# Kernel optimization log

Hardware: AMD Instinct MI355X
Metric: run time of the kernel (lower is better)

The kernel has to match this reference:

```python
import jax, jax.numpy as jnp
import numpy as np

B = 262144
I = 128  # input_size
H = 128  # hidden_size


def setup_inputs() -> dict:
    key = jax.random.key(0)
    ks = jax.random.split(key, 12)
    std = 1.0 / np.sqrt(H)
    u = lambda k, shape: jax.random.uniform(k, shape, jnp.float32, -std, std)
    return {
        "inputs": jax.random.normal(ks[0], (B, I), jnp.float32),
        "h_prev": jax.random.normal(ks[1], (B, H), jnp.float32),
        "c_prev": jax.random.normal(ks[2], (B, H), jnp.float32),
        "W_ii": u(ks[3], (H, I)), "W_hi": u(ks[4], (H, H)),
        "W_if": u(ks[5], (H, I)), "W_hf": u(ks[6], (H, H)),
        "W_io": u(ks[7], (H, I)), "W_ho": u(ks[8], (H, H)),
        "W_ig": u(ks[9], (H, I)), "W_hg": u(ks[10], (H, H)),
    }


def reference(inputs, h_prev, c_prev, W_ii, W_hi, W_if, W_hf, W_io, W_ho, W_ig, W_hg):
    # Same math as 8 separate GEMMs, expressed as 2 fused GEMMs over concatenated gates.
    W_x = jnp.concatenate([W_ii, W_if, W_io, W_ig], axis=0)  # [4H, I]
    W_h = jnp.concatenate([W_hi, W_hf, W_ho, W_hg], axis=0)  # [4H, H]
    gates = inputs @ W_x.T + h_prev @ W_h.T  # [B, 4H]
    gi, gf, go, gg = jnp.split(gates, 4, axis=-1)
    i_t = jax.nn.sigmoid(gi)
    f_t = jax.nn.sigmoid(gf)
    o_t = jax.nn.sigmoid(go)
    g_t = jnp.tanh(gg)
    c_t = f_t * c_prev + i_t * g_t
    h_t = o_t * jnp.tanh(c_t)
    return jnp.stack([h_t, c_t], axis=0)  # [2, B, H]
```

## Files before the change

kernel.cpp:

```cpp
#include <hip/hip_runtime.h>

#define BATCH 262144
#define NBLK 256
#define NITER 16
#define ASTRIDE 264
#define BH 33554432

typedef __attribute__((ext_vector_type(8))) short bf16x8;
typedef __attribute__((ext_vector_type(4))) float f32x4;
typedef __attribute__((ext_vector_type(8))) unsigned short u16x8;

__device__ __forceinline__ unsigned short f2bf(float f) {
  unsigned int u = __float_as_uint(f);
  u += 0x7fffu + ((u >> 16) & 1u);
  return (unsigned short)(u >> 16);
}

__device__ __forceinline__ float fexp(float x) { return __builtin_amdgcn_exp2f(x * 1.44269504f); }
__device__ __forceinline__ float sigm(float x) { return __builtin_amdgcn_rcpf(1.f + fexp(-x)); }
__device__ __forceinline__ float ftanh(float x) { return 1.f - 2.f * __builtin_amdgcn_rcpf(1.f + fexp(2.f * x)); }

__global__ __launch_bounds__(512, 2) void lstm_fused(
    const float* __restrict__ X, const float* __restrict__ H0, const float* __restrict__ C0,
    const float* __restrict__ Wii, const float* __restrict__ Whi,
    const float* __restrict__ Wif, const float* __restrict__ Whf,
    const float* __restrict__ Wio, const float* __restrict__ Who,
    const float* __restrict__ Wig, const float* __restrict__ Whg,
    float* __restrict__ Out) {
  __shared__ __align__(16) unsigned short Abuf[2][64 * ASTRIDE];

  const int tid = threadIdx.x;
  const int wave = tid >> 6;
  const int lane = tid & 63;
  const int lrow = lane & 15;
  const int lk = (lane >> 4) * 8;
  const int hcol = wave * 16 + lrow;
  const int r0 = tid >> 4;
  const int cc = (tid & 15) * 8;

  const float* Wxp[4] = {Wii, Wif, Wio, Wig};
  const float* Whp[4] = {Whi, Whf, Who, Whg};

  bf16x8 wf[4][8];
#pragma unroll
  for (int g = 0; g < 4; ++g) {
#pragma unroll
    for (int kk = 0; kk < 8; ++kk) {
      const int k = kk * 32 + lk;
      const float* src = (kk < 4) ? (Wxp[g] + hcol * 128 + k)
                                  : (Whp[g] + hcol * 128 + (k - 128));
      float4 lo = *(const float4*)src;
      float4 hi = *(const float4*)(src + 4);
      bf16x8 w;
      w[0] = (short)f2bf(lo.x); w[1] = (short)f2bf(lo.y);
      w[2] = (short)f2bf(lo.z); w[3] = (short)f2bf(lo.w);
      w[4] = (short)f2bf(hi.x); w[5] = (short)f2bf(hi.y);
      w[6] = (short)f2bf(hi.z); w[7] = (short)f2bf(hi.w);
      wf[g][kk] = w;
    }
  }

  float4 sx0, sx1, sx2, sx3, sh0, sh1, sh2, sh3;
  float cv[16];

#define ISSUE_LOADS(ROW0) do {                                           \
    const float* px_ = X + (size_t)((ROW0) + r0) * 128 + cc;             \
    sx0 = *(const float4*)px_;  sx1 = *(const float4*)(px_ + 4);         \
    const float* ph_ = H0 + (size_t)((ROW0) + r0) * 128 + cc;            \
    sh0 = *(const float4*)ph_;  sh1 = *(const float4*)(ph_ + 4);         \
    const float* qx_ = px_ + 32 * 128;                                   \
    sx2 = *(const float4*)qx_;  sx3 = *(const float4*)(qx_ + 4);         \
    const float* qh_ = ph_ + 32 * 128;                                   \
    sh2 = *(const float4*)qh_;  sh3 = *(const float4*)(qh_ + 4);         \
  } while (0)

#define ISSUE_CV(ROW0) do {                                              \
    const int rbv_ = (ROW0) + (lane >> 4) * 4;                           \
    _Pragma("unroll")                                                    \
    for (int mt_ = 0; mt_ < 4; ++mt_)                                    \
      _Pragma("unroll")                                                  \
      for (int j_ = 0; j_ < 4; ++j_)                                     \
        cv[mt_ * 4 + j_] = C0[(size_t)(rbv_ + mt_ * 16 + j_) * 128 + hcol]; \
  } while (0)

#define CVT8(DST, A, B) do {                                             \
    u16x8 t_;                                                            \
    t_[0] = f2bf((A).x); t_[1] = f2bf((A).y);                            \
    t_[2] = f2bf((A).z); t_[3] = f2bf((A).w);                            \
    t_[4] = f2bf((B).x); t_[5] = f2bf((B).y);                            \
    t_[6] = f2bf((B).z); t_[7] = f2bf((B).w);                            \
    *(u16x8*)(DST) = t_;                                                 \
  } while (0)

#define BODY(IT, AB) do {                                                \
    const int row0_ = (blockIdx.x + (IT) * NBLK) * 64;                   \
                              \
    CVT8(&(AB)[r0 * ASTRIDE + cc], sx0, sx1);                            \
    CVT8(&(AB)[r0 * ASTRIDE + 128 + cc], sh0, sh1);                      \
    CVT8(&(AB)[(r0 + 32) * ASTRIDE + cc], sx2, sx3);                     \
    CVT8(&(AB)[(r0 + 32) * ASTRIDE + 128 + cc], sh2, sh3);               \
    __syncthreads();        \
    \
        \
                                       \
    ISSUE_CV(row0_);                                                     \
    if ((IT) + 1 < NITER) ISSUE_LOADS(row0_ + NBLK * 64);                \
    const int rb_ = row0_ + (lane >> 4) * 4;                             \
    _Pragma("unroll")                                                    \
    for (int mt = 0; mt < 4; ++mt) {                                     \
      f32x4 a0 = {0.f, 0.f, 0.f, 0.f}, a1 = a0, a2 = a0, a3 = a0;        \
      _Pragma("unroll")                                                  \
      for (int kk = 0; kk < 8; ++kk) {                                   \
        bf16x8 a = *(const bf16x8*)&(AB)[(mt * 16 + lrow) * ASTRIDE + kk * 32 + lk]; \
        a0 = __builtin_amdgcn_mfma_f32_16x16x32_bf16(a, wf[0][kk], a0, 0, 0, 0); \
        a1 = __builtin_amdgcn_mfma_f32_16x16x32_bf16(a, wf[1][kk], a1, 0, 0, 0); \
        a2 = __builtin_amdgcn_mfma_f32_16x16x32_bf16(a, wf[2][kk], a2, 0, 0, 0); \
        a3 = __builtin_amdgcn_mfma_f32_16x16x32_bf16(a, wf[3][kk], a3, 0, 0, 0); \
      }                                                                  \
      _Pragma("unroll")                                                  \
      for (int j = 0; j < 4; ++j) {                                      \
        const int rg = rb_ + mt * 16 + j;                                \
        const float itv = sigm(a0[j]);                                   \
        const float ftv = sigm(a1[j]);                                   \
        const float otv = sigm(a2[j]);                                   \
        const float gtv = ftanh(a3[j]);                                  \
        const float ctv = ftv * cv[mt * 4 + j] + itv * gtv;              \
        const float htv = otv * ftanh(ctv);                              \
        Out[(size_t)rg * 128 + hcol] = htv;                              \
        Out[BH + (size_t)rg * 128 + hcol] = ctv;                         \
      }                                                                  \
    }                                                                    \
  } while (0)

  ISSUE_LOADS(blockIdx.x * 64);

  for (int it = 0; it < NITER; it += 2) {
    BODY(it, &Abuf[0][0]);
    BODY(it + 1, &Abuf[1][0]);
  }

#undef ISSUE_LOADS
#undef ISSUE_CV
#undef CVT8
#undef BODY
}

extern "C" void kernel_launch(void* const* d_in, const int* in_sizes, int n_in,
                              void* d_out, int out_size, void* d_ws, size_t ws_size,
                              hipStream_t stream) {
  (void)in_sizes; (void)n_in; (void)out_size; (void)d_ws; (void)ws_size;
  lstm_fused<<<NBLK, 512, 0, stream>>>(
      (const float*)d_in[0], (const float*)d_in[1], (const float*)d_in[2],
      (const float*)d_in[3], (const float*)d_in[4], (const float*)d_in[5],
      (const float*)d_in[6], (const float*)d_in[7], (const float*)d_in[8],
      (const float*)d_in[9], (const float*)d_in[10],
      (float*)d_out);
}
```

Before: 160.4 us.

## Split hidden columns across blocks and exchange gate results through LDS

Each block now covers 32 rows and half of the hidden columns, and each wave holds weights for only two gates, so register pressure drops and occupancy can rise to four blocks per CU. Gate pre-activations are written to an LDS buffer so every thread can gather all four gates for one column. This gives coalesced 64-wide stores for h and c and coalesced c_prev loads. Block-to-tile mapping is swizzled by XCD. In exchange, each block's X/H tile is loaded twice (once per column half), and every iteration gains an extra barrier plus an LDS round trip.

After: 178.8 us. 1.11x slower.

```diff
diff --git a/kernel.cpp b/kernel.cpp
--- a/kernel.cpp
+++ b/kernel.cpp
@@ -1,9 +1,12 @@
 #include <hip/hip_runtime.h>
 
 #define BATCH 262144
-#define NBLK 256
-#define NITER 16
+#define NBLK 512
+#define NITER 32
+#define ROWS 32
 #define ASTRIDE 264
+#define GSTRIDE 68
+#define GPLANE (ROWS * GSTRIDE)
 #define BH 33554432
 
 typedef __attribute__((ext_vector_type(8))) short bf16x8;
@@ -20,33 +23,43 @@
 __device__ __forceinline__ float sigm(float x) { return __builtin_amdgcn_rcpf(1.f + fexp(-x)); }
 __device__ __forceinline__ float ftanh(float x) { return 1.f - 2.f * __builtin_amdgcn_rcpf(1.f + fexp(2.f * x)); }
 
-__global__ __launch_bounds__(512, 2) void lstm_fused(
+__global__ __launch_bounds__(512, 4) void lstm_fused(
     const float* __restrict__ X, const float* __restrict__ H0, const float* __restrict__ C0,
     const float* __restrict__ Wii, const float* __restrict__ Whi,
     const float* __restrict__ Wif, const float* __restrict__ Whf,
     const float* __restrict__ Wio, const float* __restrict__ Who,
     const float* __restrict__ Wig, const float* __restrict__ Whg,
     float* __restrict__ Out) {
-  __shared__ __align__(16) unsigned short Abuf[2][64 * ASTRIDE];
+  __shared__ __align__(16) unsigned short Abuf[2][ROWS * ASTRIDE];
+  __shared__ __align__(16) float Glds[4 * GPLANE];
 
   const int tid = threadIdx.x;
   const int wave = tid >> 6;
   const int lane = tid & 63;
   const int lrow = lane & 15;
-  const int lk = (lane >> 4) * 8;
-  const int hcol = wave * 16 + lrow;
-  const int r0 = tid >> 4;
-  const int cc = (tid & 15) * 8;
+  const int lkq = lane >> 4;
+  const int ct = wave & 3;
+  const int gp = wave >> 2;
+
+  const int bid = blockIdx.x;
+  const int xcd = bid & 7;
+  const int ch = (bid >> 3) & 1;
+  const int p = bid >> 4;
+  const int tbase = p + 32 * xcd;
+  const int col0 = ch * 64;
+
+  const int hcol = col0 + ct * 16 + lrow;
 
   const float* Wxp[4] = {Wii, Wif, Wio, Wig};
   const float* Whp[4] = {Whi, Whf, Who, Whg};
 
-  bf16x8 wf[4][8];
+  bf16x8 wf[2][8];
 #pragma unroll
-  for (int g = 0; g < 4; ++g) {
+  for (int gg = 0; gg < 2; ++gg) {
+    const int g = gp * 2 + gg;
 #pragma unroll
     for (int kk = 0; kk < 8; ++kk) {
-      const int k = kk * 32 + lk;
+      const int k = kk * 32 + lkq * 8;
       const float* src = (kk < 4) ? (Wxp[g] + hcol * 128 + k)
                                   : (Whp[g] + hcol * 128 + (k - 128));
       float4 lo = *(const float4*)src;
@@ -56,83 +69,89 @@
       w[2] = (short)f2bf(lo.z); w[3] = (short)f2bf(lo.w);
       w[4] = (short)f2bf(hi.x); w[5] = (short)f2bf(hi.y);
       w[6] = (short)f2bf(hi.z); w[7] = (short)f2bf(hi.w);
-      wf[g][kk] = w;
+      wf[gg][kk] = w;
     }
   }
 
-  float4 sx0, sx1, sx2, sx3, sh0, sh1, sh2, sh3;
-  float cv[16];
+  const int r0 = tid >> 4;
+  const int ci = tid & 15;
+  float4 s0, s1, s2, s3;
+  float cva[4];
 
-#define ISSUE_LOADS(ROW0) do {                                           \
-    const float* px_ = X + (size_t)((ROW0) + r0) * 128 + cc;             \
-    sx0 = *(const float4*)px_;  sx1 = *(const float4*)(px_ + 4);         \
-    const float* ph_ = H0 + (size_t)((ROW0) + r0) * 128 + cc;            \
-    sh0 = *(const float4*)ph_;  sh1 = *(const float4*)(ph_ + 4);         \
-    const float* qx_ = px_ + 32 * 128;                                   \
-    sx2 = *(const float4*)qx_;  sx3 = *(const float4*)(qx_ + 4);         \
-    const float* qh_ = ph_ + 32 * 128;                                   \
-    sh2 = *(const float4*)qh_;  sh3 = *(const float4*)(qh_ + 4);         \
+#define ISSUE_LOADS(ROW0) do {                                            \
+    const float* b_ = (ci < 8)                                            \
+        ? (X + (size_t)((ROW0) + r0) * 128 + ci * 16)                     \
+        : (H0 + (size_t)((ROW0) + r0) * 128 + (ci - 8) * 16);             \
+    s0 = ((const float4*)b_)[0];  s1 = ((const float4*)b_)[1];            \
+    s2 = ((const float4*)b_)[2];  s3 = ((const float4*)b_)[3];            \
   } while (0)
 
-#define ISSUE_CV(ROW0) do {                                              \
-    const int rbv_ = (ROW0) + (lane >> 4) * 4;                           \
-    _Pragma("unroll")                                                    \
-    for (int mt_ = 0; mt_ < 4; ++mt_)                                    \
-      _Pragma("unroll")                                                  \
-      for (int j_ = 0; j_ < 4; ++j_)                                     \
-        cv[mt_ * 4 + j_] = C0[(size_t)(rbv_ + mt_ * 16 + j_) * 128 + hcol]; \
+#define ISSUE_CV(ROW0) do {                                               \
+    _Pragma("unroll")                                                     \
+    for (int j_ = 0; j_ < 4; ++j_)                                        \
+      cva[j_] = C0[(size_t)((ROW0) + 4 * wave + j_) * 128 + col0 + lane]; \
   } while (0)
 
-#define CVT8(DST, A, B) do {                                             \
-    u16x8 t_;                                                            \
-    t_[0] = f2bf((A).x); t_[1] = f2bf((A).y);                            \
-    t_[2] = f2bf((A).z); t_[3] = f2bf((A).w);                            \
-    t_[4] = f2bf((B).x); t_[5] = f2bf((B).y);                            \
-    t_[6] = f2bf((B).z); t_[7] = f2bf((B).w);                            \
-    *(u16x8*)(DST) = t_;                                                 \
+#define CVT8(DST, A, B) do {                                              \
+    u16x8 t_;                                                             \
+    t_[0] = f2bf((A).x); t_[1] = f2bf((A).y);                             \
+    t_[2] = f2bf((A).z); t_[3] = f2bf((A).w);                             \
+    t_[4] = f2bf((B).x); t_[5] = f2bf((B).y);                             \
+    t_[6] = f2bf((B).z); t_[7] = f2bf((B).w);                             \
+    *(u16x8*)(DST) = t_;                                                  \
   } while (0)
 
-#define BODY(IT, AB) do {                                                \
-    const int row0_ = (blockIdx.x + (IT) * NBLK) * 64;                   \
-                              \
-    CVT8(&(AB)[r0 * ASTRIDE + cc], sx0, sx1);                            \
-    CVT8(&(AB)[r0 * ASTRIDE + 128 + cc], sh0, sh1);                      \
-    CVT8(&(AB)[(r0 + 32) * ASTRIDE + cc], sx2, sx3);                     \
-    CVT8(&(AB)[(r0 + 32) * ASTRIDE + 128 + cc], sh2, sh3);               \
-    __syncthreads();        \
-    \
-        \
-                                       \
-    ISSUE_CV(row0_);                                                     \
-    if ((IT) + 1 < NITER) ISSUE_LOADS(row0_ + NBLK * 64);                \
-    const int rb_ = row0_ + (lane >> 4) * 4;                             \
-    _Pragma("unroll")                                                    \
-    for (int mt = 0; mt < 4; ++mt) {                                     \
-      f32x4 a0 = {0.f, 0.f, 0.f, 0.f}, a1 = a0, a2 = a0, a3 = a0;        \
-      _Pragma("unroll")                                                  \
-      for (int kk = 0; kk < 8; ++kk) {                                   \
-        bf16x8 a = *(const bf16x8*)&(AB)[(mt * 16 + lrow) * ASTRIDE + kk * 32 + lk]; \
-        a0 = __builtin_amdgcn_mfma_f32_16x16x32_bf16(a, wf[0][kk], a0, 0, 0, 0); \
-        a1 = __builtin_amdgcn_mfma_f32_16x16x32_bf16(a, wf[1][kk], a1, 0, 0, 0); \
-        a2 = __builtin_amdgcn_mfma_f32_16x16x32_bf16(a, wf[2][kk], a2, 0, 0, 0); \
-        a3 = __builtin_amdgcn_mfma_f32_16x16x32_bf16(a, wf[3][kk], a3, 0, 0, 0); \
-      }                                                                  \
-      _Pragma("unroll")                                                  \
-      for (int j = 0; j < 4; ++j) {                                      \
-        const int rg = rb_ + mt * 16 + j;                                \
-        const float itv = sigm(a0[j]);                                   \
-        const float ftv = sigm(a1[j]);                                   \
-        const float otv = sigm(a2[j]);                                   \
-        const float gtv = ftanh(a3[j]);                                  \
-        const float ctv = ftv * cv[mt * 4 + j] + itv * gtv;              \
-        const float htv = otv * ftanh(ctv);                              \
-        Out[(size_t)rg * 128 + hcol] = htv;                              \
-        Out[BH + (size_t)rg * 128 + hcol] = ctv;                         \
-      }                                                                  \
-    }                                                                    \
+#define BODY(IT, AB) do {                                                 \
+    const int row0_ = (tbase + (IT) * 256) * ROWS;                        \
+                                             \
+    CVT8(&(AB)[r0 * ASTRIDE + ci * 16], s0, s1);                          \
+    CVT8(&(AB)[r0 * ASTRIDE + ci * 16 + 8], s2, s3);                      \
+    __syncthreads();    \
+    ISSUE_CV(row0_);          \
+                                  \
+    f32x4 a00 = {0.f, 0.f, 0.f, 0.f}, a01 = a00, a10 = a00, a11 = a00;    \
+    _Pragma("unroll")                                                     \
+    for (int kk = 0; kk < 8; ++kk) {                                      \
+      bf16x8 aA = *(const bf16x8*)&(AB)[lrow * ASTRIDE + kk * 32 + lkq * 8];        \
+      bf16x8 aB = *(const bf16x8*)&(AB)[(16 + lrow) * ASTRIDE + kk * 32 + lkq * 8]; \
+      a00 = __builtin_amdgcn_mfma_f32_16x16x32_bf16(aA, wf[0][kk], a00, 0, 0, 0);   \
+      a01 = __builtin_amdgcn_mfma_f32_16x16x32_bf16(aA, wf[1][kk], a01, 0, 0, 0);   \
+      a10 = __builtin_amdgcn_mfma_f32_16x16x32_bf16(aB, wf[0][kk], a10, 0, 0, 0);   \
+      a11 = __builtin_amdgcn_mfma_f32_16x16x32_bf16(aB, wf[1][kk], a11, 0, 0, 0);   \
+    }                                                                     \
+                                          \
+    _Pragma("unroll")                                                     \
+    for (int j_ = 0; j_ < 4; ++j_) {                                      \
+      const int gr = (lkq * 4 + j_) * GSTRIDE + ct * 16 + lrow;           \
+      Glds[(gp * 2 + 0) * GPLANE + gr] = a00[j_];                         \
+      Glds[(gp * 2 + 1) * GPLANE + gr] = a01[j_];                         \
+      Glds[(gp * 2 + 0) * GPLANE + 16 * GSTRIDE + gr] = a10[j_];          \
+      Glds[(gp * 2 + 1) * GPLANE + 16 * GSTRIDE + gr] = a11[j_];          \
+    }                                                                     \
+    __syncthreads();                         \
+                \
+    if ((IT) + 1 < NITER) ISSUE_LOADS(row0_ + 256 * ROWS);                \
+      \
+    _Pragma("unroll")                                                     \
+    for (int j_ = 0; j_ < 4; ++j_) {                                      \
+      const int rl = 4 * wave + j_;                                       \
+      const float gi = Glds[0 * GPLANE + rl * GSTRIDE + lane];            \
+      const float gf = Glds[1 * GPLANE + rl * GSTRIDE + lane];            \
+      const float go = Glds[2 * GPLANE + rl * GSTRIDE + lane];            \
+      const float gc = Glds[3 * GPLANE + rl * GSTRIDE + lane];            \
+      const float itv = sigm(gi);                                         \
+      const float ftv = sigm(gf);                                         \
+      const float otv = sigm(go);                                         \
+      const float gtv = ftanh(gc);                                        \
+      const float ctv = ftv * cva[j_] + itv * gtv;                        \
+      const float htv = otv * ftanh(ctv);                                 \
+      const size_t o_ = (size_t)(row0_ + rl) * 128 + col0 + lane;         \
+      Out[o_] = htv;                                                      \
+      Out[BH + o_] = ctv;                                                 \
+    }                                                                     \
   } while (0)
 
-  ISSUE_LOADS(blockIdx.x * 64);
+  ISSUE_LOADS(tbase * ROWS);
 
   for (int it = 0; it < NITER; it += 2) {
     BODY(it, &Abuf[0][0]);
```
